# Kernel optimization log

Measured on AMD Instinct MI355X. Metric: run time of the kernel, lower is better.

## Reference

```python
import jax, jax.numpy as jnp
import numpy as np
import math

EPS = 1e-12  # F.normalize default eps

def _l2_normalize(x):
    n = jnp.sqrt(jnp.sum(x * x, axis=-1, keepdims=True))
    return x / jnp.maximum(n, EPS)

def setup_inputs() -> dict:
    key = jax.random.key(0)
    k1, k2 = jax.random.split(key)
    B, F, C = 16384, 1024, 1000
    features = jax.random.normal(k1, (B, F), dtype=jnp.float32)
    prototypes = jax.random.normal(k2, (C, F), dtype=jnp.float32)
    distance_scale = jnp.ones((1,), dtype=jnp.float32)
    temperature = jnp.ones((1,), dtype=jnp.float32)
    return {"features": features, "prototypes": prototypes,
            "distance_scale": distance_scale, "temperature": temperature}

def reference(features, prototypes, distance_scale, temperature):
    # L2-normalize both sides (F.normalize, p=2, eps=1e-12)
    f = _l2_normalize(features)      # [B, F]
    p = _l2_normalize(prototypes)    # [C, F]
    # Pairwise Euclidean distance. For unit vectors ||f-p||^2 = 2 - 2 f.p,
    # clamped at 0 for numerical safety; then / sqrt(2).
    sim = jnp.einsum('bf,cf->bc', f, p)                  # [B, C]
    sq = jnp.maximum(2.0 - 2.0 * sim, 0.0)
    distances = jnp.sqrt(sq) / jnp.float32(math.sqrt(2.0))
    iso = jnp.abs(distance_scale) * distances            # [B, C]
    logits = -(iso + jnp.mean(iso, axis=1, keepdims=True))
    return logits / temperature
```

## Files before the change

kernel.cpp:

```cpp
#include <hip/hip_runtime.h>
#include <hip/hip_bf16.h>
#include <math.h>

#define B_ROWS 16384
#define C_COLS 1000
#define C_PAD  1024
#define FDIM   1024
#define FBLKS  4096
#define FP8_SCALE 256.0f
#define INV_SIM   (1.0f / (FP8_SCALE * FP8_SCALE))

typedef __attribute__((ext_vector_type(8))) short bf16x8;
typedef __attribute__((ext_vector_type(4))) float f32x4;
typedef __attribute__((ext_vector_type(4))) int   i32x4;
typedef __attribute__((ext_vector_type(8))) int   i32x8;

#define GLD_LDS(gp, lp) __builtin_amdgcn_global_load_lds( \
    (__attribute__((address_space(1))) void*)(gp),        \
    (__attribute__((address_space(3))) void*)(lp), 16, 0, 0)

__global__ __launch_bounds__(256) void normalize_all(
    const float* __restrict__ feat, const float* __restrict__ prot,
    unsigned char* __restrict__ fb, unsigned char* __restrict__ pb,
    float* __restrict__ rowsum)
{
    const int lane = threadIdx.x & 63;
    const int wave = threadIdx.x >> 6;

    if (blockIdx.x < 64) rowsum[blockIdx.x * 256 + threadIdx.x] = 0.0f;

    const float* in;
    unsigned char* out;
    int row, nvalid;
    if (blockIdx.x < FBLKS) {
        row = blockIdx.x * 4 + wave;  in = feat; out = fb; nvalid = B_ROWS;
    } else {
        row = (blockIdx.x - FBLKS) * 4 + wave;  in = prot; out = pb; nvalid = C_COLS;
    }
    unsigned char* orow = out + (size_t)row * FDIM;

    if (row >= nvalid) {
        i32x4 z = {0, 0, 0, 0};
        ((i32x4*)orow)[lane] = z;
        return;
    }

    const float4* rp = (const float4*)(in + (size_t)row * FDIM);
    float4 v[4];
    float ss = 0.0f;
    #pragma unroll
    for (int c = 0; c < 4; ++c) {
        v[c] = rp[lane * 4 + c];
        ss += v[c].x * v[c].x + v[c].y * v[c].y + v[c].z * v[c].z + v[c].w * v[c].w;
    }
    #pragma unroll
    for (int off = 1; off < 64; off <<= 1) ss += __shfl_xor(ss, off, 64);
    const float inv = FP8_SCALE / sqrtf(fmaxf(ss, 1e-24f));

    i32x4 pk;
    #pragma unroll
    for (int c = 0; c < 4; ++c) {
        int w0 = __builtin_amdgcn_cvt_pk_fp8_f32(v[c].x * inv, v[c].y * inv, 0, false);
        w0     = __builtin_amdgcn_cvt_pk_fp8_f32(v[c].z * inv, v[c].w * inv, w0, true);
        pk[c] = w0;
    }
    ((i32x4*)orow)[lane] = pk;
}

__global__ __launch_bounds__(256) void gemm_dist(
    const unsigned char* __restrict__ A,
    const unsigned char* __restrict__ Bp,
    __hip_bfloat16* __restrict__ D,
    float* __restrict__ rowsum)
{
    __shared__ unsigned char As[2 * 128 * 128];
    __shared__ unsigned char Bs[2 * 128 * 128];

    const int tid  = threadIdx.x;
    const int lane = tid & 63;
    const int wave = tid >> 6;

    const int id  = blockIdx.x;
    const int xcd = id & 7;
    const int seq = id >> 3;
    const int bn  = seq & 7;
    const int bm  = xcd * 16 + (seq >> 3);

    const int waveM = (wave >> 1) * 64;
    const int waveN = (wave & 1) * 64;

    f32x4 acc[4][4] = {};

    const int srow8 = lane >> 3;
    const int sg    = (lane & 7) ^ srow8;
    const unsigned char* Abase = A  + ((size_t)(bm * 128 + wave * 8 + srow8)) * FDIM + sg * 16;
    const unsigned char* Bbase = Bp + ((size_t)(bn * 128 + wave * 8 + srow8)) * FDIM + sg * 16;

    const int q2   = (lane >> 4) * 2;
    const int bxor = lane & 7;
    const int fA = (waveM + (lane & 15)) * 128;
    const int fB = (waveN + (lane & 15)) * 128;
    const int pg0 = ((q2)     ^ bxor) * 16;
    const int pg1 = ((q2 + 1) ^ bxor) * 16;

    const int ldsRow = wave * 8 * 128;

    #pragma unroll
    for (int r = 0; r < 4; ++r) {
        GLD_LDS(Abase + (size_t)(r * 32) * FDIM, &As[ldsRow + r * 32 * 128]);
        GLD_LDS(Bbase + (size_t)(r * 32) * FDIM, &Bs[ldsRow + r * 32 * 128]);
    }
    __syncthreads();

    #pragma unroll 1
    for (int t = 0; t < 8; ++t) {
        const int cur = (t & 1) << 14;
        const int nxt = cur ^ 16384;

        if (t < 7) {
            const int k0n = (t + 1) * 128;
            #pragma unroll
            for (int r = 0; r < 4; ++r) {
                GLD_LDS(Abase + (size_t)(r * 32) * FDIM + k0n, &As[nxt + ldsRow + r * 32 * 128]);
                GLD_LDS(Bbase + (size_t)(r * 32) * FDIM + k0n, &Bs[nxt + ldsRow + r * 32 * 128]);
            }
        }

        i32x8 b[4];
        #pragma unroll
        for (int nt = 0; nt < 4; ++nt) {
            const i32x4 lo = *(const i32x4*)&Bs[cur + fB + nt * 2048 + pg0];
            const i32x4 hi = *(const i32x4*)&Bs[cur + fB + nt * 2048 + pg1];
            b[nt] = (i32x8){lo.x, lo.y, lo.z, lo.w, hi.x, hi.y, hi.z, hi.w};
        }
        #pragma unroll
        for (int mt = 0; mt < 4; ++mt) {
            const i32x4 lo = *(const i32x4*)&As[cur + fA + mt * 2048 + pg0];
            const i32x4 hi = *(const i32x4*)&As[cur + fA + mt * 2048 + pg1];
            const i32x8 a = (i32x8){lo.x, lo.y, lo.z, lo.w, hi.x, hi.y, hi.z, hi.w};
            #pragma unroll
            for (int nt = 0; nt < 4; ++nt)
                acc[mt][nt] = __builtin_amdgcn_mfma_scale_f32_16x16x128_f8f6f4(
                    a, b[nt], acc[mt][nt], 0, 0, 0, 127, 0, 127);
        }

        __syncthreads();
    }

    const int row0 = bm * 128 + waveM;
    const int col0 = bn * 128 + waveN;
    #pragma unroll
    for (int mt = 0; mt < 4; ++mt) {
        #pragma unroll
        for (int r = 0; r < 4; ++r) {
            const int row = row0 + mt * 16 + (lane >> 4) * 4 + r;
            float part = 0.0f;
            #pragma unroll
            for (int nt = 0; nt < 4; ++nt) {
                const int col = col0 + nt * 16 + (lane & 15);
                const float sim = acc[mt][nt][r] * INV_SIM;
                const float dv = sqrtf(fmaxf(1.0f - sim, 0.0f));
                if (col < C_COLS) {
                    D[(size_t)row * C_COLS + col] = __float2bfloat16(dv);
                    part += dv;
                }
            }
            part += __shfl_xor(part, 1, 64);
            part += __shfl_xor(part, 2, 64);
            part += __shfl_xor(part, 4, 64);
            part += __shfl_xor(part, 8, 64);
            if ((lane & 15) == 0) atomicAdd(&rowsum[row], part);
        }
    }
}

__global__ __launch_bounds__(256) void finalize(
    const __hip_bfloat16* __restrict__ D, const float* __restrict__ rowsum,
    const float* __restrict__ scale, const float* __restrict__ temp,
    float* __restrict__ out)
{
    const size_t i = (size_t)blockIdx.x * 256 + threadIdx.x;
    const float a = -fabsf(scale[0]) / temp[0];
    const int row = (int)((i * 8) / C_COLS);
    const float m = rowsum[row] * (1.0f / (float)C_COLS);

    const bf16x8 dv = *(const bf16x8*)(D + i * 8);
    const __hip_bfloat16* dp = (const __hip_bfloat16*)&dv;
    float4 o0, o1;
    o0.x = a * (__bfloat162float(dp[0]) + m);
    o0.y = a * (__bfloat162float(dp[1]) + m);
    o0.z = a * (__bfloat162float(dp[2]) + m);
    o0.w = a * (__bfloat162float(dp[3]) + m);
    o1.x = a * (__bfloat162float(dp[4]) + m);
    o1.y = a * (__bfloat162float(dp[5]) + m);
    o1.z = a * (__bfloat162float(dp[6]) + m);
    o1.w = a * (__bfloat162float(dp[7]) + m);
    ((float4*)out)[i * 2]     = o0;
    ((float4*)out)[i * 2 + 1] = o1;
}

extern "C" void kernel_launch(void* const* d_in, const int* in_sizes, int n_in,
                              void* d_out, int out_size, void* d_ws, size_t ws_size,
                              hipStream_t stream)
{
    const float* features = (const float*)d_in[0];
    const float* protos   = (const float*)d_in[1];
    const float* dscale   = (const float*)d_in[2];
    const float* temp     = (const float*)d_in[3];
    float* out = (float*)d_out;

    char* ws = (char*)d_ws;
    unsigned char* fb = (unsigned char*)ws;
    unsigned char* pb = (unsigned char*)(ws + 16777216);
    __hip_bfloat16* D = (__hip_bfloat16*)(ws + 17825792);
    float* rowsum     = (float*)(ws + 50593792);

    normalize_all<<<FBLKS + C_PAD / 4, 256, 0, stream>>>(features, protos, fb, pb, rowsum);

    gemm_dist<<<1024, 256, 0, stream>>>(fb, pb, D, rowsum);

    finalize<<<(B_ROWS * C_COLS / 8) / 256, 256, 0, stream>>>(D, rowsum, dscale, temp, out);
}
```

Before: 161.0 us.

## Deepen GEMM K-loop prefetch with explicit vmcnt waits and split barriers

Restructures the FP8 GEMM main loop so two K-tiles are in flight. Before the loop both LDS buffers are filled. Each iteration waits with a partial vmcnt instead of a full __syncthreads, reads all A/B fragments, issues the MFMAs at raised wave priority, then refills the just-consumed buffer two tiles ahead after a second barrier. The last tile is peeled out of the loop. This aims to hide global-to-LDS latency behind compute, at the cost of an extra barrier per iteration and hand-tuned waitcnt values that must match the number of outstanding loads.

After: 159.2 us. Within noise of the previous version (-1.1%).

```diff
diff --git a/kernel.cpp b/kernel.cpp
--- a/kernel.cpp
+++ b/kernel.cpp
@@ -110,41 +110,85 @@
         GLD_LDS(Abase + (size_t)(r * 32) * FDIM, &As[ldsRow + r * 32 * 128]);
         GLD_LDS(Bbase + (size_t)(r * 32) * FDIM, &Bs[ldsRow + r * 32 * 128]);
     }
-    __syncthreads();
+    __builtin_amdgcn_sched_barrier(0);
+    #pragma unroll
+    for (int r = 0; r < 4; ++r) {
+        GLD_LDS(Abase + (size_t)(r * 32) * FDIM + 128, &As[16384 + ldsRow + r * 32 * 128]);
+        GLD_LDS(Bbase + (size_t)(r * 32) * FDIM + 128, &Bs[16384 + ldsRow + r * 32 * 128]);
+    }
+    __builtin_amdgcn_sched_barrier(0);
 
     #pragma unroll 1
-    for (int t = 0; t < 8; ++t) {
+    for (int t = 0; t < 7; ++t) {
+        asm volatile("s_waitcnt vmcnt(8)" ::: "memory");
+        __builtin_amdgcn_s_barrier();
+        __builtin_amdgcn_sched_barrier(0);
+
         const int cur = (t & 1) << 14;
-        const int nxt = cur ^ 16384;
-
-        if (t < 7) {
-            const int k0n = (t + 1) * 128;
-            #pragma unroll
-            for (int r = 0; r < 4; ++r) {
-                GLD_LDS(Abase + (size_t)(r * 32) * FDIM + k0n, &As[nxt + ldsRow + r * 32 * 128]);
-                GLD_LDS(Bbase + (size_t)(r * 32) * FDIM + k0n, &Bs[nxt + ldsRow + r * 32 * 128]);
-            }
-        }
-
-        i32x8 b[4];
+
+        i32x8 a4[4], b4[4];
         #pragma unroll
         for (int nt = 0; nt < 4; ++nt) {
             const i32x4 lo = *(const i32x4*)&Bs[cur + fB + nt * 2048 + pg0];
             const i32x4 hi = *(const i32x4*)&Bs[cur + fB + nt * 2048 + pg1];
-            b[nt] = (i32x8){lo.x, lo.y, lo.z, lo.w, hi.x, hi.y, hi.z, hi.w};
+            b4[nt] = (i32x8){lo.x, lo.y, lo.z, lo.w, hi.x, hi.y, hi.z, hi.w};
         }
         #pragma unroll
         for (int mt = 0; mt < 4; ++mt) {
             const i32x4 lo = *(const i32x4*)&As[cur + fA + mt * 2048 + pg0];
             const i32x4 hi = *(const i32x4*)&As[cur + fA + mt * 2048 + pg1];
-            const i32x8 a = (i32x8){lo.x, lo.y, lo.z, lo.w, hi.x, hi.y, hi.z, hi.w};
+            a4[mt] = (i32x8){lo.x, lo.y, lo.z, lo.w, hi.x, hi.y, hi.z, hi.w};
+        }
+
+        __builtin_amdgcn_s_setprio(1);
+        #pragma unroll
+        for (int mt = 0; mt < 4; ++mt)
             #pragma unroll
             for (int nt = 0; nt < 4; ++nt)
                 acc[mt][nt] = __builtin_amdgcn_mfma_scale_f32_16x16x128_f8f6f4(
-                    a, b[nt], acc[mt][nt], 0, 0, 0, 127, 0, 127);
-        }
-
-        __syncthreads();
+                    a4[mt], b4[nt], acc[mt][nt], 0, 0, 0, 127, 0, 127);
+        __builtin_amdgcn_s_setprio(0);
+
+        if (t < 6) {
+            asm volatile("s_waitcnt lgkmcnt(0)" ::: "memory");
+            __builtin_amdgcn_s_barrier();
+            __builtin_amdgcn_sched_barrier(0);
+            const int k0n = (t + 2) * 128;
+            #pragma unroll
+            for (int r = 0; r < 4; ++r) {
+                GLD_LDS(Abase + (size_t)(r * 32) * FDIM + k0n, &As[cur + ldsRow + r * 32 * 128]);
+                GLD_LDS(Bbase + (size_t)(r * 32) * FDIM + k0n, &Bs[cur + ldsRow + r * 32 * 128]);
+            }
+            __builtin_amdgcn_sched_barrier(0);
+        }
+    }
+
+    asm volatile("s_waitcnt vmcnt(0)" ::: "memory");
+    __builtin_amdgcn_s_barrier();
+    __builtin_amdgcn_sched_barrier(0);
+    {
+        const int cur = 16384;
+        i32x8 a4[4], b4[4];
+        #pragma unroll
+        for (int nt = 0; nt < 4; ++nt) {
+            const i32x4 lo = *(const i32x4*)&Bs[cur + fB + nt * 2048 + pg0];
+            const i32x4 hi = *(const i32x4*)&Bs[cur + fB + nt * 2048 + pg1];
+            b4[nt] = (i32x8){lo.x, lo.y, lo.z, lo.w, hi.x, hi.y, hi.z, hi.w};
+        }
+        #pragma unroll
+        for (int mt = 0; mt < 4; ++mt) {
+            const i32x4 lo = *(const i32x4*)&As[cur + fA + mt * 2048 + pg0];
+            const i32x4 hi = *(const i32x4*)&As[cur + fA + mt * 2048 + pg1];
+            a4[mt] = (i32x8){lo.x, lo.y, lo.z, lo.w, hi.x, hi.y, hi.z, hi.w};
+        }
+        __builtin_amdgcn_s_setprio(1);
+        #pragma unroll
+        for (int mt = 0; mt < 4; ++mt)
+            #pragma unroll
+            for (int nt = 0; nt < 4; ++nt)
+                acc[mt][nt] = __builtin_amdgcn_mfma_scale_f32_16x16x128_f8f6f4(
+                    a4[mt], b4[nt], acc[mt][nt], 0, 0, 0, 127, 0, 127);
+        __builtin_amdgcn_s_setprio(0);
     }
 
     const int row0 = bm * 128 + waveM;
```
